# Optimization experiments

Hardware: AMD Instinct MI355X
Metric: run time of the kernel (lower is better)

Reference implementation:

```python
import jax, jax.numpy as jnp
import numpy as np

CLIP = 10.0

def setup_inputs() -> dict:
    key = jax.random.key(0)
    ks = jax.random.split(key, 4)
    N, C, D, H = 1024, 128, 128, 128
    s1 = 1.0 / np.sqrt(C + D)
    s2 = 1.0 / np.sqrt(H)
    return {
        "z_c": jax.random.normal(ks[0], (N, C), jnp.float32),
        "z_d": jax.random.normal(ks[1], (N, D), jnp.float32),
        "w1": jax.random.normal(ks[2], (C + D, H), jnp.float32) * s1,
        "b1": jnp.zeros((H,), jnp.float32),
        "w2": jax.random.normal(ks[3], (H,), jnp.float32) * s2,
        "b2": jnp.zeros((), jnp.float32),
    }

def reference(z_c, z_d, w1, b1, w2, b2):
    # T1[i, j] = net(concat(z_c[j], z_d[i]))  -- from zc_tile/zd_tile repeat pattern.
    # Decompose the first linear: concat([zc, zd]) @ w1 == zc @ w1[:C] + zd @ w1[C:]
    N, C = z_c.shape
    wc, wd = w1[:C], w1[C:]
    a = z_c @ wc  # [N, H], indexed by column j
    b = z_d @ wd  # [N, H], indexed by row i
    h = jax.nn.relu(a[None, :, :] + b[:, None, :] + b1)  # [N, N, H]
    T1 = h @ w2 + b2  # [N, N]
    T0 = jnp.mean(jnp.diagonal(T1))
    T1c = jnp.clip(T1, -CLIP, CLIP)
    # logmeanexp over all off-diagonal entries (diag masked to -inf)
    masked = jnp.where(jnp.eye(N, dtype=bool), -jnp.inf, T1c)
    lme = jax.nn.logsumexp(masked) - jnp.log(jnp.asarray(N * (N - 1.0), jnp.float32))
    dv = T0 - lme
    return dv
```

## Files before the change

kernel.cpp:

```cpp
#include <hip/hip_runtime.h>
#include <math.h>

#define N 1024
#define H 128
#define CLIPV 10.0f

#define TI 64
#define TJ 64
#define LDSP 132
#define NBLK ((N / TI) * (N / TJ))

__global__ __launch_bounds__(256) void k_gemm(const float* __restrict__ z_c,
                                              const float* __restrict__ z_d,
                                              const float* __restrict__ w1,
                                              const float* __restrict__ b1,
                                              float* __restrict__ A,
                                              float* __restrict__ Cb) {
    const int which = blockIdx.y;
    const int n0 = blockIdx.x * 8;
    const int tid = threadIdx.x;
    const float* __restrict__ z = which ? z_d : z_c;
    const float* __restrict__ w = w1 + which * (H * H);

    __shared__ float zs[8][H];
    {
        const int c4 = (tid & 31) * 4;
        const int r  = tid >> 5;
        *(float4*)&zs[r][c4] = *(const float4*)&z[(n0 + r) * H + c4];
    }
    __syncthreads();

    const int h = tid & 127;
    const int g = tid >> 7;

    float a0 = 0.f, a1 = 0.f, a2 = 0.f, a3 = 0.f;
    #pragma unroll 8
    for (int k = 0; k < H; ++k) {
        const float wv = w[k * H + h];
        a0 = fmaf(zs[g * 4 + 0][k], wv, a0);
        a1 = fmaf(zs[g * 4 + 1][k], wv, a1);
        a2 = fmaf(zs[g * 4 + 2][k], wv, a2);
        a3 = fmaf(zs[g * 4 + 3][k], wv, a3);
    }
    const float bias = which ? b1[h] : 0.0f;
    float* __restrict__ dst = which ? Cb : A;
    dst[(n0 + g * 4 + 0) * H + h] = a0 + bias;
    dst[(n0 + g * 4 + 1) * H + h] = a1 + bias;
    dst[(n0 + g * 4 + 2) * H + h] = a2 + bias;
    dst[(n0 + g * 4 + 3) * H + h] = a3 + bias;
}

__global__ __launch_bounds__(512, 1) void k_pair(const float* __restrict__ A,
                                                 const float* __restrict__ Cb,
                                                 const float* __restrict__ w2,
                                                 const float* __restrict__ b2p,
                                                 float* __restrict__ pdiag,
                                                 float* __restrict__ psume) {
    __shared__ float Ash[TJ][LDSP];
    __shared__ float Csh[TI][LDSP];
    __shared__ float w2s[H];
    __shared__ float red[16];

    const int tid = threadIdx.x;
    const int i0 = blockIdx.x * TI;
    const int j0 = blockIdx.y * TJ;

    {
        const int c4 = (tid & 31) * 4;
        const int r  = tid >> 5;
        #pragma unroll
        for (int rr = 0; rr < 4; ++rr) {
            const int row = r + rr * 16;
            *(float4*)&Ash[row][c4] = *(const float4*)&A[(j0 + row) * H + c4];
            *(float4*)&Csh[row][c4] = *(const float4*)&Cb[(i0 + row) * H + c4];
        }
        if (tid < 32) *(float4*)&w2s[tid * 4] = *(const float4*)&w2[tid * 4];
    }
    __syncthreads();

    const int t256 = tid & 255;
    const int tj = t256 & 15;
    const int ti = t256 >> 4;
    const int hh = tid >> 8;

    float s[4][4] = {{0.f,0.f,0.f,0.f},{0.f,0.f,0.f,0.f},
                     {0.f,0.f,0.f,0.f},{0.f,0.f,0.f,0.f}};

    const int h4base = hh * 16;
    #pragma unroll 4
    for (int h4i = 0; h4i < 16; ++h4i) {
        const int h4 = h4base + h4i;
        const float4 w4 = *(const float4*)&w2s[h4 * 4];
        float4 cf[4], af[4];
        #pragma unroll
        for (int d = 0; d < 4; ++d) {
            cf[d] = *(const float4*)&Csh[ti + d * 16][h4 * 4];
            af[d] = *(const float4*)&Ash[tj + d * 16][h4 * 4];
        }
        #pragma unroll
        for (int q = 0; q < 4; ++q) {
            const float wv = ((const float*)&w4)[q];
            #pragma unroll
            for (int di = 0; di < 4; ++di) {
                const float cv = ((const float*)&cf[di])[q];
                #pragma unroll
                for (int dj = 0; dj < 4; ++dj) {
                    const float t = fmaxf(cv + ((const float*)&af[dj])[q], 0.f);
                    s[di][dj] = fmaf(t, wv, s[di][dj]);
                }
            }
        }
    }

    float* comb = &Ash[0][0];
    __syncthreads();
    if (hh == 1) {
        #pragma unroll
        for (int di = 0; di < 4; ++di) {
            float4 v4;
            v4.x = s[di][0]; v4.y = s[di][1]; v4.z = s[di][2]; v4.w = s[di][3];
            *(float4*)&comb[t256 * 20 + di * 4] = v4;
        }
    }
    __syncthreads();

    float diag = 0.f, sume = 0.f;
    if (hh == 0) {
        const float b2 = b2p[0];
        #pragma unroll
        for (int di = 0; di < 4; ++di) {
            #pragma unroll
            for (int dj = 0; dj < 4; ++dj) {
                const float v = s[di][dj] + comb[t256 * 20 + di * 4 + dj] + b2;
                const int i = i0 + ti + di * 16;
                const int j = j0 + tj + dj * 16;
                if (i == j) {
                    diag += v;
                } else {
                    const float vc = fminf(fmaxf(v, -CLIPV), CLIPV);
                    sume += __expf(vc - CLIPV);
                }
            }
        }
    }

    #pragma unroll
    for (int off = 32; off; off >>= 1) {
        diag += __shfl_down(diag, off);
        sume += __shfl_down(sume, off);
    }
    if ((tid & 63) == 0) { red[tid >> 6] = diag; red[8 + (tid >> 6)] = sume; }
    __syncthreads();
    if (tid == 0) {
        float d = 0.f, e = 0.f;
        #pragma unroll
        for (int k = 0; k < 8; ++k) { d += red[k]; e += red[8 + k]; }
        const int bid = blockIdx.y * gridDim.x + blockIdx.x;
        pdiag[bid] = d;
        psume[bid] = e;
    }
}

__global__ __launch_bounds__(256) void k_final(const float* __restrict__ pdiag,
                                               const float* __restrict__ psume,
                                               float* __restrict__ out) {
    const int tid = threadIdx.x;
    double d = (double)pdiag[tid];
    double e = (double)psume[tid];
    #pragma unroll
    for (int off = 32; off; off >>= 1) {
        d += __shfl_down(d, off);
        e += __shfl_down(e, off);
    }
    __shared__ double rd[4], re[4];
    if ((tid & 63) == 0) { rd[tid >> 6] = d; re[tid >> 6] = e; }
    __syncthreads();
    if (tid == 0) {
        const double dt = rd[0] + rd[1] + rd[2] + rd[3];
        const double et = re[0] + re[1] + re[2] + re[3];
        const double T0  = dt / (double)N;
        const double lme = log(et) + (double)CLIPV
                         - log((double)N * ((double)N - 1.0));
        out[0] = (float)(T0 - lme);
    }
}

extern "C" void kernel_launch(void* const* d_in, const int* in_sizes, int n_in,
                              void* d_out, int out_size, void* d_ws, size_t ws_size,
                              hipStream_t stream) {
    const float* z_c = (const float*)d_in[0];
    const float* z_d = (const float*)d_in[1];
    const float* w1  = (const float*)d_in[2];
    const float* b1  = (const float*)d_in[3];
    const float* w2  = (const float*)d_in[4];
    const float* b2  = (const float*)d_in[5];

    float* A     = (float*)d_ws;
    float* Cb    = A + N * H;
    float* pdiag = Cb + N * H;
    float* psume = pdiag + NBLK;

    k_gemm<<<dim3(N / 8, 2), 256, 0, stream>>>(z_c, z_d, w1, b1, A, Cb);
    k_pair<<<dim3(N / TI, N / TJ), 512, 0, stream>>>(A, Cb, w2, b2, pdiag, psume);
    k_final<<<1, 256, 0, stream>>>(pdiag, psume, (float*)d_out);
}
```

Before: 82.79 us.

## Split hidden dim four ways, halve pair tile, fuse final reduction via atomics

The pair kernel tile shrinks from 64x64 to 64x32 and the hidden dimension is split across four thread groups instead of two, with partial sums combined through shared memory. This doubles the block count to 512 so more CUs are busy. The separate final-reduction kernel is removed: each block atomically adds double partials, and the last block (found with a counter) computes the output. The first GEMM is rewritten without shared memory, reads z rows directly, and zeroes the accumulators. The costs are more cross-group reduction traffic, atomic contention, and a GEMM with less register reuse.

```diff
diff --git a/kernel.cpp b/kernel.cpp
--- a/kernel.cpp
+++ b/kernel.cpp
@@ -6,60 +6,51 @@
 #define CLIPV 10.0f
 
 #define TI 64
-#define TJ 64
+#define TJ 32
 #define LDSP 132
-#define NBLK ((N / TI) * (N / TJ))
+#define GRID_I (N / TI)
+#define GRID_J (N / TJ)
+#define NBLK (GRID_I * GRID_J)
 
-__global__ __launch_bounds__(256) void k_gemm(const float* __restrict__ z_c,
+__global__ __launch_bounds__(512) void k_gemm(const float* __restrict__ z_c,
                                               const float* __restrict__ z_d,
                                               const float* __restrict__ w1,
                                               const float* __restrict__ b1,
                                               float* __restrict__ A,
-                                              float* __restrict__ Cb) {
-    const int which = blockIdx.y;
-    const int n0 = blockIdx.x * 8;
+                                              float* __restrict__ Cb,
+                                              double* __restrict__ acc,
+                                              int* __restrict__ counter) {
     const int tid = threadIdx.x;
-    const float* __restrict__ z = which ? z_d : z_c;
-    const float* __restrict__ w = w1 + which * (H * H);
+    if (blockIdx.x == 0 && tid == 0) {
+        acc[0] = 0.0; acc[1] = 0.0; *counter = 0;
+    }
+    const int gid = blockIdx.x * 512 + tid;
+    const int row = gid >> 7;
+    const int h   = gid & 127;
+    const float* __restrict__ zc = z_c + row * H;
+    const float* __restrict__ zd = z_d + row * H;
 
-    __shared__ float zs[8][H];
-    {
-        const int c4 = (tid & 31) * 4;
-        const int r  = tid >> 5;
-        *(float4*)&zs[r][c4] = *(const float4*)&z[(n0 + r) * H + c4];
-    }
-    __syncthreads();
-
-    const int h = tid & 127;
-    const int g = tid >> 7;
-
-    float a0 = 0.f, a1 = 0.f, a2 = 0.f, a3 = 0.f;
+    float a = 0.f, c = 0.f;
     #pragma unroll 8
     for (int k = 0; k < H; ++k) {
-        const float wv = w[k * H + h];
-        a0 = fmaf(zs[g * 4 + 0][k], wv, a0);
-        a1 = fmaf(zs[g * 4 + 1][k], wv, a1);
-        a2 = fmaf(zs[g * 4 + 2][k], wv, a2);
-        a3 = fmaf(zs[g * 4 + 3][k], wv, a3);
+        a = fmaf(zc[k], w1[k * H + h],       a);
+        c = fmaf(zd[k], w1[(H + k) * H + h], c);
     }
-    const float bias = which ? b1[h] : 0.0f;
-    float* __restrict__ dst = which ? Cb : A;
-    dst[(n0 + g * 4 + 0) * H + h] = a0 + bias;
-    dst[(n0 + g * 4 + 1) * H + h] = a1 + bias;
-    dst[(n0 + g * 4 + 2) * H + h] = a2 + bias;
-    dst[(n0 + g * 4 + 3) * H + h] = a3 + bias;
+    A[row * H + h]  = a;
+    Cb[row * H + h] = c + b1[h];
 }
 
 __global__ __launch_bounds__(512, 1) void k_pair(const float* __restrict__ A,
                                                  const float* __restrict__ Cb,
                                                  const float* __restrict__ w2,
                                                  const float* __restrict__ b2p,
-                                                 float* __restrict__ pdiag,
-                                                 float* __restrict__ psume) {
+                                                 double* __restrict__ acc,
+                                                 int* __restrict__ counter,
+                                                 float* __restrict__ out) {
     __shared__ float Ash[TJ][LDSP];
     __shared__ float Csh[TI][LDSP];
     __shared__ float w2s[H];
-    __shared__ float red[16];
+    __shared__ float red[4];
 
     const int tid = threadIdx.x;
     const int i0 = blockIdx.x * TI;
@@ -68,34 +59,33 @@
     {
         const int c4 = (tid & 31) * 4;
         const int r  = tid >> 5;
-        #pragma unroll
-        for (int rr = 0; rr < 4; ++rr) {
-            const int row = r + rr * 16;
-            *(float4*)&Ash[row][c4] = *(const float4*)&A[(j0 + row) * H + c4];
-            *(float4*)&Csh[row][c4] = *(const float4*)&Cb[(i0 + row) * H + c4];
-        }
+        *(float4*)&Csh[r     ][c4] = *(const float4*)&Cb[(i0 + r     ) * H + c4];
+        *(float4*)&Csh[r + 16][c4] = *(const float4*)&Cb[(i0 + r + 16) * H + c4];
+        *(float4*)&Csh[r + 32][c4] = *(const float4*)&Cb[(i0 + r + 32) * H + c4];
+        *(float4*)&Csh[r + 48][c4] = *(const float4*)&Cb[(i0 + r + 48) * H + c4];
+        *(float4*)&Ash[r     ][c4] = *(const float4*)&A [(j0 + r     ) * H + c4];
+        *(float4*)&Ash[r + 16][c4] = *(const float4*)&A [(j0 + r + 16) * H + c4];
         if (tid < 32) *(float4*)&w2s[tid * 4] = *(const float4*)&w2[tid * 4];
     }
     __syncthreads();
 
-    const int t256 = tid & 255;
-    const int tj = t256 & 15;
-    const int ti = t256 >> 4;
-    const int hh = tid >> 8;
+    const int t128 = tid & 127;
+    const int hh = tid >> 7;
+    const int tj = t128 & 7;
+    const int ti = t128 >> 3;
 
     float s[4][4] = {{0.f,0.f,0.f,0.f},{0.f,0.f,0.f,0.f},
                      {0.f,0.f,0.f,0.f},{0.f,0.f,0.f,0.f}};
 
-    const int h4base = hh * 16;
     #pragma unroll 4
-    for (int h4i = 0; h4i < 16; ++h4i) {
-        const int h4 = h4base + h4i;
+    for (int h4i = 0; h4i < 8; ++h4i) {
+        const int h4 = hh * 8 + h4i;
         const float4 w4 = *(const float4*)&w2s[h4 * 4];
         float4 cf[4], af[4];
         #pragma unroll
         for (int d = 0; d < 4; ++d) {
             cf[d] = *(const float4*)&Csh[ti + d * 16][h4 * 4];
-            af[d] = *(const float4*)&Ash[tj + d * 16][h4 * 4];
+            af[d] = *(const float4*)&Ash[tj + d * 8 ][h4 * 4];
         }
         #pragma unroll
         for (int q = 0; q < 4; ++q) {
@@ -112,14 +102,17 @@
         }
     }
 
-    float* comb = &Ash[0][0];
     __syncthreads();
-    if (hh == 1) {
+    float* scr1 = &Ash[0][0];
+    float* scr2 = &Csh[0][0];
+    float* scr3 = &Csh[0][0] + 2192;
+    if (hh != 0) {
+        float* dst = (hh == 1) ? scr1 : (hh == 2) ? scr2 : scr3;
         #pragma unroll
         for (int di = 0; di < 4; ++di) {
             float4 v4;
             v4.x = s[di][0]; v4.y = s[di][1]; v4.z = s[di][2]; v4.w = s[di][3];
-            *(float4*)&comb[t256 * 20 + di * 4] = v4;
+            *(float4*)&dst[t128 * 17 + di * 4] = v4;
         }
     }
     __syncthreads();
@@ -129,11 +122,15 @@
         const float b2 = b2p[0];
         #pragma unroll
         for (int di = 0; di < 4; ++di) {
+            const float4 p1 = *(const float4*)&scr1[t128 * 17 + di * 4];
+            const float4 p2 = *(const float4*)&scr2[t128 * 17 + di * 4];
+            const float4 p3 = *(const float4*)&scr3[t128 * 17 + di * 4];
             #pragma unroll
             for (int dj = 0; dj < 4; ++dj) {
-                const float v = s[di][dj] + comb[t256 * 20 + di * 4 + dj] + b2;
+                const float v = s[di][dj] + ((const float*)&p1)[dj]
+                              + ((const float*)&p2)[dj] + ((const float*)&p3)[dj] + b2;
                 const int i = i0 + ti + di * 16;
-                const int j = j0 + tj + dj * 16;
+                const int j = j0 + tj + dj * 8;
                 if (i == j) {
                     diag += v;
                 } else {
@@ -149,39 +146,22 @@
         diag += __shfl_down(diag, off);
         sume += __shfl_down(sume, off);
     }
-    if ((tid & 63) == 0) { red[tid >> 6] = diag; red[8 + (tid >> 6)] = sume; }
+    if (tid == 0)  { red[0] = diag; red[2] = sume; }
+    if (tid == 64) { red[1] = diag; red[3] = sume; }
     __syncthreads();
     if (tid == 0) {
-        float d = 0.f, e = 0.f;
-        #pragma unroll
-        for (int k = 0; k < 8; ++k) { d += red[k]; e += red[8 + k]; }
-        const int bid = blockIdx.y * gridDim.x + blockIdx.x;
-        pdiag[bid] = d;
-        psume[bid] = e;
-    }
-}
-
-__global__ __launch_bounds__(256) void k_final(const float* __restrict__ pdiag,
-                                               const float* __restrict__ psume,
-                                               float* __restrict__ out) {
-    const int tid = threadIdx.x;
-    double d = (double)pdiag[tid];
-    double e = (double)psume[tid];
-    #pragma unroll
-    for (int off = 32; off; off >>= 1) {
-        d += __shfl_down(d, off);
-        e += __shfl_down(e, off);
-    }
-    __shared__ double rd[4], re[4];
-    if ((tid & 63) == 0) { rd[tid >> 6] = d; re[tid >> 6] = e; }
-    __syncthreads();
-    if (tid == 0) {
-        const double dt = rd[0] + rd[1] + rd[2] + rd[3];
-        const double et = re[0] + re[1] + re[2] + re[3];
-        const double T0  = dt / (double)N;
-        const double lme = log(et) + (double)CLIPV
-                         - log((double)N * ((double)N - 1.0));
-        out[0] = (float)(T0 - lme);
+        atomicAdd(&acc[0], (double)(red[0] + red[1]));
+        atomicAdd(&acc[1], (double)(red[2] + red[3]));
+        __threadfence();
+        const int old = atomicAdd(counter, 1);
+        if (old == NBLK - 1) {
+            const double dt = atomicAdd(&acc[0], 0.0);
+            const double et = atomicAdd(&acc[1], 0.0);
+            const double T0  = dt / (double)N;
+            const double lme = log(et) + (double)CLIPV
+                             - log((double)N * ((double)N - 1.0));
+            out[0] = (float)(T0 - lme);
+        }
     }
 }
 
@@ -195,12 +175,12 @@
     const float* w2  = (const float*)d_in[4];
     const float* b2  = (const float*)d_in[5];
 
-    float* A     = (float*)d_ws;
-    float* Cb    = A + N * H;
-    float* pdiag = Cb + N * H;
-    float* psume = pdiag + NBLK;
+    float*  A       = (float*)d_ws;
+    float*  Cb      = A + N * H;
+    double* acc     = (double*)(Cb + N * H);
+    int*    counter = (int*)(acc + 2);
 
-    k_gemm<<<dim3(N / 8, 2), 256, 0, stream>>>(z_c, z_d, w1, b1, A, Cb);
-    k_pair<<<dim3(N / TI, N / TJ), 512, 0, stream>>>(A, Cb, w2, b2, pdiag, psume);
-    k_final<<<1, 256, 0, stream>>>(pdiag, psume, (float*)d_out);
+    k_gemm<<<dim3(256), 512, 0, stream>>>(z_c, z_d, w1, b1, A, Cb, acc, counter);
+    k_pair<<<dim3(GRID_I, GRID_J), 512, 0, stream>>>(A, Cb, w2, b2, acc, counter,
+                                                     (float*)d_out);
 }
```

New measurement: 100.6 us. +21.5%, slower.

## Reshape pair kernel to 4x8 register tiles with four-way H split

Applied to the files above, without the earlier changes.

The pair kernel now gives each thread a 4x8 output tile over a quarter of the hidden dimension, instead of a 4x4 tile over half. The four H-partials are combined through three LDS scratch regions. This raises arithmetic per LDS load (12 float4 loads per 128 FMA-pairs, up from 8 per 64) but uses more accumulator registers and adds an extra reduction stage. The gemm kernel also moves to 512 threads with 2 rows per thread, for more parallelism per block.

```diff
diff --git a/kernel.cpp b/kernel.cpp
--- a/kernel.cpp
+++ b/kernel.cpp
@@ -10,7 +10,7 @@
 #define LDSP 132
 #define NBLK ((N / TI) * (N / TJ))
 
-__global__ __launch_bounds__(256) void k_gemm(const float* __restrict__ z_c,
+__global__ __launch_bounds__(512) void k_gemm(const float* __restrict__ z_c,
                                               const float* __restrict__ z_d,
                                               const float* __restrict__ w1,
                                               const float* __restrict__ b1,
@@ -23,7 +23,7 @@
     const float* __restrict__ w = w1 + which * (H * H);
 
     __shared__ float zs[8][H];
-    {
+    if (tid < 256) {
         const int c4 = (tid & 31) * 4;
         const int r  = tid >> 5;
         *(float4*)&zs[r][c4] = *(const float4*)&z[(n0 + r) * H + c4];
@@ -33,21 +33,17 @@
     const int h = tid & 127;
     const int g = tid >> 7;
 
-    float a0 = 0.f, a1 = 0.f, a2 = 0.f, a3 = 0.f;
+    float a0 = 0.f, a1 = 0.f;
     #pragma unroll 8
     for (int k = 0; k < H; ++k) {
         const float wv = w[k * H + h];
-        a0 = fmaf(zs[g * 4 + 0][k], wv, a0);
-        a1 = fmaf(zs[g * 4 + 1][k], wv, a1);
-        a2 = fmaf(zs[g * 4 + 2][k], wv, a2);
-        a3 = fmaf(zs[g * 4 + 3][k], wv, a3);
+        a0 = fmaf(zs[2 * g + 0][k], wv, a0);
+        a1 = fmaf(zs[2 * g + 1][k], wv, a1);
     }
     const float bias = which ? b1[h] : 0.0f;
     float* __restrict__ dst = which ? Cb : A;
-    dst[(n0 + g * 4 + 0) * H + h] = a0 + bias;
-    dst[(n0 + g * 4 + 1) * H + h] = a1 + bias;
-    dst[(n0 + g * 4 + 2) * H + h] = a2 + bias;
-    dst[(n0 + g * 4 + 3) * H + h] = a3 + bias;
+    dst[(n0 + 2 * g + 0) * H + h] = a0 + bias;
+    dst[(n0 + 2 * g + 1) * H + h] = a1 + bias;
 }
 
 __global__ __launch_bounds__(512, 1) void k_pair(const float* __restrict__ A,
@@ -78,25 +74,29 @@
     }
     __syncthreads();
 
-    const int t256 = tid & 255;
-    const int tj = t256 & 15;
-    const int ti = t256 >> 4;
-    const int hh = tid >> 8;
-
-    float s[4][4] = {{0.f,0.f,0.f,0.f},{0.f,0.f,0.f,0.f},
-                     {0.f,0.f,0.f,0.f},{0.f,0.f,0.f,0.f}};
-
-    const int h4base = hh * 16;
-    #pragma unroll 4
-    for (int h4i = 0; h4i < 16; ++h4i) {
+    const int t128 = tid & 127;
+    const int hh = tid >> 7;
+    const int tj = t128 & 7;
+    const int ti = t128 >> 3;
+
+    float s[4][8];
+    #pragma unroll
+    for (int di = 0; di < 4; ++di)
+        #pragma unroll
+        for (int dj = 0; dj < 8; ++dj) s[di][dj] = 0.f;
+
+    const int h4base = hh * 8;
+    #pragma unroll 2
+    for (int h4i = 0; h4i < 8; ++h4i) {
         const int h4 = h4base + h4i;
         const float4 w4 = *(const float4*)&w2s[h4 * 4];
-        float4 cf[4], af[4];
-        #pragma unroll
-        for (int d = 0; d < 4; ++d) {
+        float4 cf[4], af[8];
+        #pragma unroll
+        for (int d = 0; d < 4; ++d)
             cf[d] = *(const float4*)&Csh[ti + d * 16][h4 * 4];
-            af[d] = *(const float4*)&Ash[tj + d * 16][h4 * 4];
-        }
+        #pragma unroll
+        for (int e = 0; e < 8; ++e)
+            af[e] = *(const float4*)&Ash[tj + e * 8][h4 * 4];
         #pragma unroll
         for (int q = 0; q < 4; ++q) {
             const float wv = ((const float*)&w4)[q];
@@ -104,7 +104,7 @@
             for (int di = 0; di < 4; ++di) {
                 const float cv = ((const float*)&cf[di])[q];
                 #pragma unroll
-                for (int dj = 0; dj < 4; ++dj) {
+                for (int dj = 0; dj < 8; ++dj) {
                     const float t = fmaxf(cv + ((const float*)&af[dj])[q], 0.f);
                     s[di][dj] = fmaf(t, wv, s[di][dj]);
                 }
@@ -112,14 +112,19 @@
         }
     }
 
-    float* comb = &Ash[0][0];
-    __syncthreads();
-    if (hh == 1) {
+    __syncthreads();
+    float* scr1 = &Ash[0][0];
+    float* scr2 = &Csh[0][0];
+    float* scr3 = &Csh[0][0] + 4224;
+    if (hh != 0) {
+        float* dst = (hh == 1) ? scr1 : (hh == 2) ? scr2 : scr3;
         #pragma unroll
         for (int di = 0; di < 4; ++di) {
-            float4 v4;
-            v4.x = s[di][0]; v4.y = s[di][1]; v4.z = s[di][2]; v4.w = s[di][3];
-            *(float4*)&comb[t256 * 20 + di * 4] = v4;
+            float4 lo, hi;
+            lo.x = s[di][0]; lo.y = s[di][1]; lo.z = s[di][2]; lo.w = s[di][3];
+            hi.x = s[di][4]; hi.y = s[di][5]; hi.z = s[di][6]; hi.w = s[di][7];
+            *(float4*)&dst[((di * 2 + 0) * 128 + t128) * 4] = lo;
+            *(float4*)&dst[((di * 2 + 1) * 128 + t128) * 4] = hi;
         }
     }
     __syncthreads();
@@ -130,15 +135,25 @@
         #pragma unroll
         for (int di = 0; di < 4; ++di) {
             #pragma unroll
-            for (int dj = 0; dj < 4; ++dj) {
-                const float v = s[di][dj] + comb[t256 * 20 + di * 4 + dj] + b2;
-                const int i = i0 + ti + di * 16;
-                const int j = j0 + tj + dj * 16;
-                if (i == j) {
-                    diag += v;
-                } else {
-                    const float vc = fminf(fmaxf(v, -CLIPV), CLIPV);
-                    sume += __expf(vc - CLIPV);
+            for (int half = 0; half < 2; ++half) {
+                const int p = di * 2 + half;
+                const float4 p1 = *(const float4*)&scr1[(p * 128 + t128) * 4];
+                const float4 p2 = *(const float4*)&scr2[(p * 128 + t128) * 4];
+                const float4 p3 = *(const float4*)&scr3[(p * 128 + t128) * 4];
+                #pragma unroll
+                for (int q = 0; q < 4; ++q) {
+                    const int dj = half * 4 + q;
+                    const float v = s[di][dj] + ((const float*)&p1)[q]
+                                  + ((const float*)&p2)[q]
+                                  + ((const float*)&p3)[q] + b2;
+                    const int i = i0 + ti + di * 16;
+                    const int j = j0 + tj + dj * 8;
+                    if (i == j) {
+                        diag += v;
+                    } else {
+                        const float vc = fminf(fmaxf(v, -CLIPV), CLIPV);
+                        sume += __expf(vc - CLIPV);
+                    }
                 }
             }
         }
@@ -200,7 +215,7 @@
     float* pdiag = Cb + N * H;
     float* psume = pdiag + NBLK;
 
-    k_gemm<<<dim3(N / 8, 2), 256, 0, stream>>>(z_c, z_d, w1, b1, A, Cb);
+    k_gemm<<<dim3(N / 8, 2), 512, 0, stream>>>(z_c, z_d, w1, b1, A, Cb);
     k_pair<<<dim3(N / TI, N / TJ), 512, 0, stream>>>(A, Cb, w2, b2, pdiag, psume);
     k_final<<<1, 256, 0, stream>>>(pdiag, psume, (float*)d_out);
 }
```

Result: no change. 83.27 us (+0.6%).
